# Kernel tuning notes

Measured on AMD Instinct MI355X. Metric: run time of the kernel, lower is better.

The kernel has to match this reference:

```python
import jax, jax.numpy as jnp
import numpy as np

N_NODES = 100000


def gcn_conv(x, W, b, src, dst, n_nodes):
    # PyG GCNConv: h = x @ W; add self-loops; sym-normalized scatter-add; + bias
    loop = jnp.arange(n_nodes, dtype=src.dtype)
    src2 = jnp.concatenate([src, loop])
    dst2 = jnp.concatenate([dst, loop])
    deg = jax.ops.segment_sum(jnp.ones(src2.shape, x.dtype), dst2, num_segments=n_nodes)
    dinv = jax.lax.rsqrt(deg)  # deg >= 1 thanks to self-loops
    norm = dinv[src2] * dinv[dst2]                 # [E+N]
    h = x @ W                                      # [N, out]
    msg = h[src2] * norm[:, None]                  # gather + scale, [E+N, out]
    out = jax.ops.segment_sum(msg, dst2, num_segments=n_nodes)  # scatter-add
    return out + b


def setup_inputs() -> dict:
    key = jax.random.key(0)
    k1, k2, k3, k4, k5 = jax.random.split(key, 5)
    nfeat, nhid = 128, 64
    n_edges = 1600000
    x = jax.random.normal(k1, (N_NODES, nfeat), dtype=jnp.float32)
    edge_index = jax.random.randint(k2, (2, n_edges), 0, N_NODES, dtype=jnp.int64)
    W1 = jax.random.normal(k3, (nfeat, nhid), dtype=jnp.float32) / np.sqrt(nfeat)
    b1 = jnp.zeros((nhid,), jnp.float32)
    W2 = jax.random.normal(k4, (nhid, nhid), dtype=jnp.float32) / np.sqrt(nhid)
    b2 = jnp.zeros((nhid,), jnp.float32)
    return {"x": x, "edge_index": edge_index, "W1": W1, "b1": b1, "W2": W2, "b2": b2}


def reference(x, edge_index, W1, b1, W2, b2):
    # eval mode: dropout is identity
    src, dst = edge_index[0], edge_index[1]
    h = jax.nn.relu(gcn_conv(x, W1, b1, src, dst, N_NODES))
    residual = h
    out = jax.nn.relu(gcn_conv(h, W2, b2, src, dst, N_NODES))
    return out + residual
```

## Files before the change

kernel.cpp:

```cpp
#include <hip/hip_runtime.h>

#define N_NODES 100000
#define NDUMMY 100000
#define NH 64
#define NB 512
#define NPB 196
#define BCAP 4096
#define PBCAP 5760
#define EPB 8192


__device__ __forceinline__ unsigned short f2bf(float f) {
    union { float f; unsigned int i; } c;
    c.f = f;
    unsigned int b = c.i;
    b += 0x7FFFu + ((b >> 16) & 1u);
    return (unsigned short)(b >> 16);
}

__device__ __forceinline__ unsigned pack2bf(float lo, float hi) {
    return (unsigned)f2bf(lo) | ((unsigned)f2bf(hi) << 16);
}

__device__ __forceinline__ float bfLO(unsigned u) {
    union { unsigned i; float f; } c; c.i = u << 16; return c.f;
}
__device__ __forceinline__ float bfHI(unsigned u) {
    union { unsigned i; float f; } c; c.i = u & 0xFFFF0000u; return c.f;
}


__global__ __launch_bounds__(512) void k_init(int* __restrict__ bcur, unsigned* __restrict__ dummy_row) {
    int t = threadIdx.x;
    if (t < NB) bcur[t] = 0;
    if (t < 32) dummy_row[t] = 0;
}


__global__ __launch_bounds__(1024) void k_sort(const int* __restrict__ src, const int* __restrict__ dst,
                                               int* __restrict__ bcur, unsigned* __restrict__ ebuf, int e) {
    __shared__ unsigned sorted[EPB];
    __shared__ unsigned short cellof[EPB];
    __shared__ int lh[NB];
    __shared__ int lbase[NB];
    __shared__ int lcur[NB];
    __shared__ int gpos[NB];
    __shared__ int wsum[8];
    const int t = threadIdx.x;
    const int e0 = blockIdx.x * EPB;
    int cnt = e - e0; if (cnt > EPB) cnt = EPB;

    if (t < NB) lh[t] = 0;
    __syncthreads();

    for (int i = t * 4; i < cnt; i += 4096) {
        int4 d4 = *(const int4*)&dst[e0 + i];
        atomicAdd(&lh[d4.x / NPB], 1);
        atomicAdd(&lh[d4.y / NPB], 1);
        atomicAdd(&lh[d4.z / NPB], 1);
        atomicAdd(&lh[d4.w / NPB], 1);
    }
    __syncthreads();

    const int lane = t & 63, wave = t >> 6;
    int v = 0, inc = 0;
    if (t < NB) {
        v = lh[t];
        inc = v;
#pragma unroll
        for (int d = 1; d < 64; d <<= 1) {
            int u = __shfl_up(inc, d, 64);
            if (lane >= d) inc += u;
        }
        if (lane == 63) wsum[wave] = inc;
    }
    __syncthreads();
    if (t < NB) {
        int woff = 0;
#pragma unroll
        for (int w = 0; w < 8; ++w)
            if (w < wave) woff += wsum[w];
        const int excl = woff + inc - v;
        lbase[t] = excl;
        lcur[t] = excl;
        gpos[t] = atomicAdd(&bcur[t], v);
    }
    __syncthreads();

    for (int i = t * 4; i < cnt; i += 4096) {
        int4 d4 = *(const int4*)&dst[e0 + i];
        int4 s4 = *(const int4*)&src[e0 + i];
        int b0 = d4.x / NPB, b1 = d4.y / NPB, b2 = d4.z / NPB, b3 = d4.w / NPB;
        int p0 = atomicAdd(&lcur[b0], 1);
        int p1 = atomicAdd(&lcur[b1], 1);
        int p2 = atomicAdd(&lcur[b2], 1);
        int p3 = atomicAdd(&lcur[b3], 1);
        sorted[p0] = ((unsigned)(d4.x - b0 * NPB) << 17) | (unsigned)s4.x; cellof[p0] = (unsigned short)b0;
        sorted[p1] = ((unsigned)(d4.y - b1 * NPB) << 17) | (unsigned)s4.y; cellof[p1] = (unsigned short)b1;
        sorted[p2] = ((unsigned)(d4.z - b2 * NPB) << 17) | (unsigned)s4.z; cellof[p2] = (unsigned short)b2;
        sorted[p3] = ((unsigned)(d4.w - b3 * NPB) << 17) | (unsigned)s4.w; cellof[p3] = (unsigned short)b3;
    }
    __syncthreads();

    for (int i = t * 4; i < cnt; i += 4096) {
        uint4 sv = *(const uint4*)&sorted[i];
        ushort4 cv = *(const ushort4*)&cellof[i];
        int c0 = cv.x, c1 = cv.y, c2 = cv.z, c3 = cv.w;
        int g0 = gpos[c0] + (i + 0 - lbase[c0]);
        int g1 = gpos[c1] + (i + 1 - lbase[c1]);
        int g2 = gpos[c2] + (i + 2 - lbase[c2]);
        int g3 = gpos[c3] + (i + 3 - lbase[c3]);
        if (g0 < BCAP) ebuf[(long long)c0 * BCAP + g0] = sv.x;
        if (g1 < BCAP) ebuf[(long long)c1 * BCAP + g1] = sv.y;
        if (g2 < BCAP) ebuf[(long long)c2 * BCAP + g2] = sv.z;
        if (g3 < BCAP) ebuf[(long long)c3 * BCAP + g3] = sv.w;
    }
}

__global__ __launch_bounds__(256) void k_build(const unsigned* __restrict__ ebuf, const int* __restrict__ bcur,
                                               int* __restrict__ rowptr, int* __restrict__ degp,
                                               float* __restrict__ dinv, int* __restrict__ csrc, int n) {
    __shared__ unsigned ls[BCAP];
    __shared__ int lh[256];
    __shared__ int lpv[256];
    __shared__ int lstart[256];
    __shared__ int lc[256];
    __shared__ int wsum[4];
    const int b = blockIdx.x;
    const int t = threadIdx.x;
    const int node0 = b * NPB;
    int count = bcur[b];
    if (count > BCAP) count = BCAP;
    const int rbase = b * PBCAP;

    lh[t] = 0;
    for (int i = t; i < count; i += 256) ls[i] = ebuf[(long long)b * BCAP + i];
    __syncthreads();
    for (int i = t; i < count; i += 256) atomicAdd(&lh[ls[i] >> 17], 1);
    __syncthreads();

    const int v = lh[t];
    lpv[t] = (v + 7) & ~7;
    __syncthreads();
    const int g = t & ~3;
    const int pvg = max(max(lpv[g], lpv[g + 1]), max(lpv[g + 2], lpv[g + 3]));

    const int lane = t & 63, wave = t >> 6;
    int inc = pvg;
#pragma unroll
    for (int d = 1; d < 64; d <<= 1) {
        int u = __shfl_up(inc, d, 64);
        if (lane >= d) inc += u;
    }
    if (lane == 63) wsum[wave] = inc;
    __syncthreads();
    int woff = 0;
#pragma unroll
    for (int w = 0; w < 4; ++w)
        if (w < wave) woff += wsum[w];
    const int start = rbase + woff + inc - pvg;

    lstart[t] = start;
    lc[t] = start;
    const int node = node0 + t;
    if (t < NPB && node < n) {
        rowptr[node] = start;
        degp[node] = pvg;
        dinv[node] = rsqrtf((float)(v + 1));
    }
    __syncthreads();

    for (int i = t; i < count; i += 256) {
        unsigned u = ls[i];
        int pos = atomicAdd(&lc[u >> 17], 1);
        csrc[pos] = (int)(u & 0x1FFFFu);
    }
    __syncthreads();

    const int pend = lstart[t] + pvg;
    for (int p = lc[t]; p < pend; ++p) csrc[p] = NDUMMY;
}


typedef __attribute__((ext_vector_type(8))) short bf16x8;
typedef __attribute__((ext_vector_type(4))) float f32x4;

template <int K>
__global__ __launch_bounds__(256, 3) void k_gemm_mfma(const float* __restrict__ X, const float* __restrict__ W,
                                                      const float* __restrict__ dinv,
                                                      unsigned short* __restrict__ out, int n) {
    constexpr int KP = K + 8;
    constexpr int NKS = K / 32;
    __shared__ unsigned short xs[128][KP];
    const int tid = threadIdx.x;
    const int lane = tid & 63;
    const int wv = tid >> 6;
    const int n0 = blockIdx.x * 128;
    const int col = lane & 15;
    const int krow = (lane >> 4) * 8;

    for (int idx = tid * 4; idx < 128 * K; idx += 1024) {
        int row = idx / K, c = idx % K;
        float4 v = make_float4(0.f, 0.f, 0.f, 0.f);
        if (n0 + row < n) v = *(const float4*)&X[(long long)(n0 + row) * K + c];
        ushort4 o;
        o.x = f2bf(v.x); o.y = f2bf(v.y); o.z = f2bf(v.z); o.w = f2bf(v.w);
        *(ushort4*)&xs[row][c] = o;
    }

    union FragU { bf16x8 v; unsigned u[4]; };
    bf16x8 wb[4][NKS];
#pragma unroll
    for (int nt = 0; nt < 4; ++nt) {
#pragma unroll
        for (int ks = 0; ks < NKS; ++ks) {
            FragU f;
#pragma unroll
            for (int m = 0; m < 4; ++m) {
                int k = ks * 32 + krow + 2 * m;
                int c = nt * 16 + col;
                f.u[m] = pack2bf(W[k * NH + c], W[(k + 1) * NH + c]);
            }
            wb[nt][ks] = f.v;
        }
    }
    __syncthreads();

    f32x4 zero = {0.f, 0.f, 0.f, 0.f};
    f32x4 acc[2][4];
#pragma unroll
    for (int mt = 0; mt < 2; ++mt)
#pragma unroll
        for (int nt = 0; nt < 4; ++nt) acc[mt][nt] = zero;

#pragma unroll
    for (int ks = 0; ks < NKS; ++ks) {
#pragma unroll
        for (int mt = 0; mt < 2; ++mt) {
            const int r = wv * 32 + mt * 16 + col;
            bf16x8 a = *(const bf16x8*)&xs[r][ks * 32 + krow];
#pragma unroll
            for (int nt = 0; nt < 4; ++nt)
                acc[mt][nt] = __builtin_amdgcn_mfma_f32_16x16x32_bf16(a, wb[nt][ks], acc[mt][nt], 0, 0, 0);
        }
    }

#pragma unroll
    for (int mt = 0; mt < 2; ++mt) {
#pragma unroll
        for (int r = 0; r < 4; ++r) {
            int node = n0 + wv * 32 + mt * 16 + (lane >> 4) * 4 + r;
            if (node < n) {
                float dv = dinv[node];
#pragma unroll
                for (int nt = 0; nt < 4; ++nt)
                    out[(long long)node * NH + nt * 16 + col] = f2bf(acc[mt][nt][r] * dv);
            }
        }
    }
}


__global__ __launch_bounds__(256) void k_agg(const unsigned* __restrict__ hs32, const float* __restrict__ dinv,
                                             const int* __restrict__ rowptr, const int* __restrict__ degp,
                                             const int* __restrict__ csrc,
                                             const float* __restrict__ bias, const float* __restrict__ resid,
                                             float* __restrict__ out, int n) {
    const int gt = blockIdx.x * 256 + threadIdx.x;
    const int wave = gt >> 6;
    const int lane = threadIdx.x & 63;
    const int sub = lane >> 4;
    const int li = lane & 15;
    const int node = wave * 4 + sub;
    if (node >= n) return;

    const uint2* hsv = (const uint2*)hs32;
    uint2 su = hsv[node * 16 + li];
    float aLx = bfLO(su.x), aHx = bfHI(su.x), aLy = bfLO(su.y), aHy = bfHI(su.y);
    float bLx = 0.f, bHx = 0.f, bLy = 0.f, bHy = 0.f;

    const int rp = rowptr[node];
    const int dg = degp[node];
    for (int e = 0; e < dg; e += 8) {
        int4 c0 = *(const int4*)&csrc[rp + e];
        int4 c1 = *(const int4*)&csrc[rp + e + 4];
        uint2 u0 = hsv[c0.x * 16 + li];
        uint2 u1 = hsv[c0.y * 16 + li];
        uint2 u2 = hsv[c0.z * 16 + li];
        uint2 u3 = hsv[c0.w * 16 + li];
        uint2 u4 = hsv[c1.x * 16 + li];
        uint2 u5 = hsv[c1.y * 16 + li];
        uint2 u6 = hsv[c1.z * 16 + li];
        uint2 u7 = hsv[c1.w * 16 + li];
        aLx += bfLO(u0.x); aHx += bfHI(u0.x); aLy += bfLO(u0.y); aHy += bfHI(u0.y);
        bLx += bfLO(u1.x); bHx += bfHI(u1.x); bLy += bfLO(u1.y); bHy += bfHI(u1.y);
        aLx += bfLO(u2.x); aHx += bfHI(u2.x); aLy += bfLO(u2.y); aHy += bfHI(u2.y);
        bLx += bfLO(u3.x); bHx += bfHI(u3.x); bLy += bfLO(u3.y); bHy += bfHI(u3.y);
        aLx += bfLO(u4.x); aHx += bfHI(u4.x); aLy += bfLO(u4.y); aHy += bfHI(u4.y);
        bLx += bfLO(u5.x); bHx += bfHI(u5.x); bLy += bfLO(u5.y); bHy += bfHI(u5.y);
        aLx += bfLO(u6.x); aHx += bfHI(u6.x); aLy += bfLO(u6.y); aHy += bfHI(u6.y);
        bLx += bfLO(u7.x); bHx += bfHI(u7.x); bLy += bfLO(u7.y); bHy += bfHI(u7.y);
    }
    const float dv = dinv[node];
    const float4 bb = *(const float4*)&bias[4 * li];
    float v0 = fmaxf(dv * (aLx + bLx) + bb.x, 0.f);
    float v1 = fmaxf(dv * (aHx + bHx) + bb.y, 0.f);
    float v2 = fmaxf(dv * (aLy + bLy) + bb.z, 0.f);
    float v3 = fmaxf(dv * (aHy + bHy) + bb.w, 0.f);
    const long long ob = (long long)node * NH + 4 * li;
    if (resid) {
        float4 rr = *(const float4*)&resid[ob];
        v0 += rr.x; v1 += rr.y; v2 += rr.z; v3 += rr.w;
    }
    *(float4*)&out[ob] = make_float4(v0, v1, v2, v3);
}


extern "C" void kernel_launch(void* const* d_in, const int* in_sizes, int n_in,
                              void* d_out, int out_size, void* d_ws, size_t ws_size,
                              hipStream_t stream) {
    const float* x  = (const float*)d_in[0];
    const int*   ei = (const int*)d_in[1];
    const float* W1 = (const float*)d_in[2];
    const float* b1 = (const float*)d_in[3];
    const float* W2 = (const float*)d_in[4];
    const float* b2 = (const float*)d_in[5];
    float* out = (float*)d_out;

    const int N = N_NODES;
    const int E = in_sizes[1] / 2;
    const int* src = ei;
    const int* dst = ei + E;

    const int NP = 100352;
    int*   bcur   = (int*)d_ws;
    int*   rowptr = bcur + NB;
    int*   degp   = rowptr + NP;
    float* dinv   = (float*)(degp + NP);
    int*   csrc   = (int*)(dinv + NP);
    unsigned* ebuf = (unsigned*)(csrc + NB * PBCAP);
    unsigned* hs32 = ebuf;
    unsigned short* hsb = (unsigned short*)hs32;
    float* h1     = (float*)(hs32 + (long long)(NDUMMY + 1) * 32);

    const int nb_sort = (E + EPB - 1) / EPB;

    k_init<<<1, 512, 0, stream>>>(bcur, hs32 + (long long)NDUMMY * 32);
    k_sort<<<nb_sort, 1024, 0, stream>>>(src, dst, bcur, ebuf, E);
    k_build<<<NB, 256, 0, stream>>>(ebuf, bcur, rowptr, degp, dinv, csrc, N);

    k_gemm_mfma<128><<<(N + 127) / 128, 256, 0, stream>>>(x, W1, dinv, hsb, N);
    k_agg<<<(N + 15) / 16, 256, 0, stream>>>(hs32, dinv, rowptr, degp, csrc, b1, nullptr, h1, N);

    k_gemm_mfma<64><<<(N + 127) / 128, 256, 0, stream>>>(h1, W2, dinv, hsb, N);
    k_agg<<<(N + 15) / 16, 256, 0, stream>>>(hs32, dinv, rowptr, degp, csrc, b2, h1, out, N);
}
```

Baseline: 135.3 us.

## Widen aggregation gathers to 16-byte rows, pad CSR groups of 8, prefetch indices

The aggregation kernel now gives each node 8 lanes that load uint4 (8 bf16 features) per neighbour instead of 16 lanes loading uint2. This halves the lanes per node and doubles the nodes per wave. Column indices for the next 8 edges are loaded one iteration ahead to hide index latency. Bucketing changes to 500 buckets of 200 nodes, and degree padding is now shared across groups of 8 nodes instead of 4, which may add more dummy-edge work.

```diff
diff --git a/kernel.cpp b/kernel.cpp
--- a/kernel.cpp
+++ b/kernel.cpp
@@ -3,10 +3,10 @@
 #define N_NODES 100000
 #define NDUMMY 100000
 #define NH 64
-#define NB 512
-#define NPB 196
+#define NB 500
+#define NPB 200
 #define BCAP 4096
-#define PBCAP 5760
+#define PBCAP 6400
 #define EPB 8192
 
 
@@ -41,16 +41,16 @@
                                                int* __restrict__ bcur, unsigned* __restrict__ ebuf, int e) {
     __shared__ unsigned sorted[EPB];
     __shared__ unsigned short cellof[EPB];
-    __shared__ int lh[NB];
-    __shared__ int lbase[NB];
-    __shared__ int lcur[NB];
-    __shared__ int gpos[NB];
+    __shared__ int lh[512];
+    __shared__ int lbase[512];
+    __shared__ int lcur[512];
+    __shared__ int gpos[512];
     __shared__ int wsum[8];
     const int t = threadIdx.x;
     const int e0 = blockIdx.x * EPB;
     int cnt = e - e0; if (cnt > EPB) cnt = EPB;
 
-    if (t < NB) lh[t] = 0;
+    if (t < 512) lh[t] = 0;
     __syncthreads();
 
     for (int i = t * 4; i < cnt; i += 4096) {
@@ -64,8 +64,8 @@
 
     const int lane = t & 63, wave = t >> 6;
     int v = 0, inc = 0;
-    if (t < NB) {
-        v = lh[t];
+    if (t < 512) {
+        v = (t < NB) ? lh[t] : 0;
         inc = v;
 #pragma unroll
         for (int d = 1; d < 64; d <<= 1) {
@@ -142,8 +142,10 @@
     const int v = lh[t];
     lpv[t] = (v + 7) & ~7;
     __syncthreads();
-    const int g = t & ~3;
-    const int pvg = max(max(lpv[g], lpv[g + 1]), max(lpv[g + 2], lpv[g + 3]));
+    const int g = t & ~7;
+    int pvg = lpv[g];
+#pragma unroll
+    for (int j = 1; j < 8; ++j) pvg = max(pvg, lpv[g + j]);
 
     const int lane = t & 63, wave = t >> 6;
     int inc = pvg;
@@ -269,50 +271,75 @@
     const int gt = blockIdx.x * 256 + threadIdx.x;
     const int wave = gt >> 6;
     const int lane = threadIdx.x & 63;
-    const int sub = lane >> 4;
-    const int li = lane & 15;
-    const int node = wave * 4 + sub;
+    const int sub = lane >> 3;
+    const int li = lane & 7;
+    const int node = wave * 8 + sub;
     if (node >= n) return;
 
-    const uint2* hsv = (const uint2*)hs32;
-    uint2 su = hsv[node * 16 + li];
-    float aLx = bfLO(su.x), aHx = bfHI(su.x), aLy = bfLO(su.y), aHy = bfHI(su.y);
-    float bLx = 0.f, bHx = 0.f, bLy = 0.f, bHy = 0.f;
+    const uint4* hsv = (const uint4*)hs32;
+    uint4 su = hsv[node * 8 + li];
+    float a0 = bfLO(su.x), a1 = bfHI(su.x), a2 = bfLO(su.y), a3 = bfHI(su.y);
+    float a4 = bfLO(su.z), a5 = bfHI(su.z), a6 = bfLO(su.w), a7 = bfHI(su.w);
+    float b0 = 0.f, b1 = 0.f, b2 = 0.f, b3 = 0.f, b4 = 0.f, b5 = 0.f, b6 = 0.f, b7 = 0.f;
 
     const int rp = rowptr[node];
     const int dg = degp[node];
+    int4 c0, c1;
+    if (dg > 0) {
+        c0 = *(const int4*)&csrc[rp];
+        c1 = *(const int4*)&csrc[rp + 4];
+    }
     for (int e = 0; e < dg; e += 8) {
-        int4 c0 = *(const int4*)&csrc[rp + e];
-        int4 c1 = *(const int4*)&csrc[rp + e + 4];
-        uint2 u0 = hsv[c0.x * 16 + li];
-        uint2 u1 = hsv[c0.y * 16 + li];
-        uint2 u2 = hsv[c0.z * 16 + li];
-        uint2 u3 = hsv[c0.w * 16 + li];
-        uint2 u4 = hsv[c1.x * 16 + li];
-        uint2 u5 = hsv[c1.y * 16 + li];
-        uint2 u6 = hsv[c1.z * 16 + li];
-        uint2 u7 = hsv[c1.w * 16 + li];
-        aLx += bfLO(u0.x); aHx += bfHI(u0.x); aLy += bfLO(u0.y); aHy += bfHI(u0.y);
-        bLx += bfLO(u1.x); bHx += bfHI(u1.x); bLy += bfLO(u1.y); bHy += bfHI(u1.y);
-        aLx += bfLO(u2.x); aHx += bfHI(u2.x); aLy += bfLO(u2.y); aHy += bfHI(u2.y);
-        bLx += bfLO(u3.x); bHx += bfHI(u3.x); bLy += bfLO(u3.y); bHy += bfHI(u3.y);
-        aLx += bfLO(u4.x); aHx += bfHI(u4.x); aLy += bfLO(u4.y); aHy += bfHI(u4.y);
-        bLx += bfLO(u5.x); bHx += bfHI(u5.x); bLy += bfLO(u5.y); bHy += bfHI(u5.y);
-        aLx += bfLO(u6.x); aHx += bfHI(u6.x); aLy += bfLO(u6.y); aHy += bfHI(u6.y);
-        bLx += bfLO(u7.x); bHx += bfHI(u7.x); bLy += bfLO(u7.y); bHy += bfHI(u7.y);
+        const int4 m0 = c0, m1 = c1;
+        if (e + 8 < dg) {
+            c0 = *(const int4*)&csrc[rp + e + 8];
+            c1 = *(const int4*)&csrc[rp + e + 12];
+        }
+        uint4 u0 = hsv[m0.x * 8 + li];
+        uint4 u1 = hsv[m0.y * 8 + li];
+        uint4 u2 = hsv[m0.z * 8 + li];
+        uint4 u3 = hsv[m0.w * 8 + li];
+        uint4 u4 = hsv[m1.x * 8 + li];
+        uint4 u5 = hsv[m1.y * 8 + li];
+        uint4 u6 = hsv[m1.z * 8 + li];
+        uint4 u7 = hsv[m1.w * 8 + li];
+        a0 += bfLO(u0.x); a1 += bfHI(u0.x); a2 += bfLO(u0.y); a3 += bfHI(u0.y);
+        a4 += bfLO(u0.z); a5 += bfHI(u0.z); a6 += bfLO(u0.w); a7 += bfHI(u0.w);
+        b0 += bfLO(u1.x); b1 += bfHI(u1.x); b2 += bfLO(u1.y); b3 += bfHI(u1.y);
+        b4 += bfLO(u1.z); b5 += bfHI(u1.z); b6 += bfLO(u1.w); b7 += bfHI(u1.w);
+        a0 += bfLO(u2.x); a1 += bfHI(u2.x); a2 += bfLO(u2.y); a3 += bfHI(u2.y);
+        a4 += bfLO(u2.z); a5 += bfHI(u2.z); a6 += bfLO(u2.w); a7 += bfHI(u2.w);
+        b0 += bfLO(u3.x); b1 += bfHI(u3.x); b2 += bfLO(u3.y); b3 += bfHI(u3.y);
+        b4 += bfLO(u3.z); b5 += bfHI(u3.z); b6 += bfLO(u3.w); b7 += bfHI(u3.w);
+        a0 += bfLO(u4.x); a1 += bfHI(u4.x); a2 += bfLO(u4.y); a3 += bfHI(u4.y);
+        a4 += bfLO(u4.z); a5 += bfHI(u4.z); a6 += bfLO(u4.w); a7 += bfHI(u4.w);
+        b0 += bfLO(u5.x); b1 += bfHI(u5.x); b2 += bfLO(u5.y); b3 += bfHI(u5.y);
+        b4 += bfLO(u5.z); b5 += bfHI(u5.z); b6 += bfLO(u5.w); b7 += bfHI(u5.w);
+        a0 += bfLO(u6.x); a1 += bfHI(u6.x); a2 += bfLO(u6.y); a3 += bfHI(u6.y);
+        a4 += bfLO(u6.z); a5 += bfHI(u6.z); a6 += bfLO(u6.w); a7 += bfHI(u6.w);
+        b0 += bfLO(u7.x); b1 += bfHI(u7.x); b2 += bfLO(u7.y); b3 += bfHI(u7.y);
+        b4 += bfLO(u7.z); b5 += bfHI(u7.z); b6 += bfLO(u7.w); b7 += bfHI(u7.w);
     }
     const float dv = dinv[node];
-    const float4 bb = *(const float4*)&bias[4 * li];
-    float v0 = fmaxf(dv * (aLx + bLx) + bb.x, 0.f);
-    float v1 = fmaxf(dv * (aHx + bHx) + bb.y, 0.f);
-    float v2 = fmaxf(dv * (aLy + bLy) + bb.z, 0.f);
-    float v3 = fmaxf(dv * (aHy + bHy) + bb.w, 0.f);
-    const long long ob = (long long)node * NH + 4 * li;
+    const float4 ba = *(const float4*)&bias[8 * li];
+    const float4 bb = *(const float4*)&bias[8 * li + 4];
+    float v0 = fmaxf(dv * (a0 + b0) + ba.x, 0.f);
+    float v1 = fmaxf(dv * (a1 + b1) + ba.y, 0.f);
+    float v2 = fmaxf(dv * (a2 + b2) + ba.z, 0.f);
+    float v3 = fmaxf(dv * (a3 + b3) + ba.w, 0.f);
+    float v4 = fmaxf(dv * (a4 + b4) + bb.x, 0.f);
+    float v5 = fmaxf(dv * (a5 + b5) + bb.y, 0.f);
+    float v6 = fmaxf(dv * (a6 + b6) + bb.z, 0.f);
+    float v7 = fmaxf(dv * (a7 + b7) + bb.w, 0.f);
+    const long long ob = (long long)node * NH + 8 * li;
     if (resid) {
-        float4 rr = *(const float4*)&resid[ob];
-        v0 += rr.x; v1 += rr.y; v2 += rr.z; v3 += rr.w;
+        float4 r0 = *(const float4*)&resid[ob];
+        float4 r1 = *(const float4*)&resid[ob + 4];
+        v0 += r0.x; v1 += r0.y; v2 += r0.z; v3 += r0.w;
+        v4 += r1.x; v5 += r1.y; v6 += r1.z; v7 += r1.w;
     }
     *(float4*)&out[ob] = make_float4(v0, v1, v2, v3);
+    *(float4*)&out[ob + 4] = make_float4(v4, v5, v6, v7);
 }
 
 
@@ -334,7 +361,7 @@
 
     const int NP = 100352;
     int*   bcur   = (int*)d_ws;
-    int*   rowptr = bcur + NB;
+    int*   rowptr = bcur + 512;
     int*   degp   = rowptr + NP;
     float* dinv   = (float*)(degp + NP);
     int*   csrc   = (int*)(dinv + NP);
@@ -350,8 +377,8 @@
     k_build<<<NB, 256, 0, stream>>>(ebuf, bcur, rowptr, degp, dinv, csrc, N);
 
     k_gemm_mfma<128><<<(N + 127) / 128, 256, 0, stream>>>(x, W1, dinv, hsb, N);
-    k_agg<<<(N + 15) / 16, 256, 0, stream>>>(hs32, dinv, rowptr, degp, csrc, b1, nullptr, h1, N);
+    k_agg<<<(N + 31) / 32, 256, 0, stream>>>(hs32, dinv, rowptr, degp, csrc, b1, nullptr, h1, N);
 
     k_gemm_mfma<64><<<(N + 127) / 128, 256, 0, stream>>>(h1, W2, dinv, hsb, N);
-    k_agg<<<(N + 15) / 16, 256, 0, stream>>>(hs32, dinv, rowptr, degp, csrc, b2, h1, out, N);
-}
+    k_agg<<<(N + 31) / 32, 256, 0, stream>>>(hs32, dinv, rowptr, degp, csrc, b2, h1, out, N);
+}
```

After: 134.0 us. Within noise of the previous version (-1.0%).
